# Kernel tuning notes

Hardware: AMD Instinct MI355X
Metric: run time of the kernel (lower is better)

Reference implementation:

```python
import jax, jax.numpy as jnp
import numpy as np

N_NODES = 50000
N_EDGES = 1_600_000
IN_C = 512
OUT_C = 10


def setup_inputs() -> dict:
    key = jax.random.key(0)
    ks = jax.random.split(key, 12)

    def glorot(k, fan_in, fan_out):
        lim = float(np.sqrt(6.0 / (fan_in + fan_out)))
        return jax.random.uniform(k, (fan_in, fan_out), jnp.float32, -lim, lim)

    x = jax.random.normal(ks[0], (N_NODES, IN_C), jnp.float32)
    edge_index = jax.random.randint(ks[1], (2, N_EDGES), 0, N_NODES, dtype=jnp.int64)
    return {
        "x": x,
        "edge_index": edge_index,
        "W1": glorot(ks[2], IN_C, 1024), "b1": jnp.zeros((1024,), jnp.float32),
        "W2": glorot(ks[3], 1024, 512), "b2": jnp.zeros((512,), jnp.float32),
        "W3": glorot(ks[4], 512, 128), "b3": jnp.zeros((128,), jnp.float32),
        "Wfc": glorot(ks[5], 128, OUT_C), "bfc": jnp.zeros((OUT_C,), jnp.float32),
    }


def gcn_conv(x, W, b, src, dst, norm, num_nodes):
    # GCNConv: out = D^{-1/2} (A + I) D^{-1/2} X W + b
    xw = x @ W  # [N, out_c]
    msg = xw[src] * norm[:, None]  # gather + scale per edge (incl. self-loops)
    out = jax.ops.segment_sum(msg, dst, num_segments=num_nodes)
    return out + b


def _build_sym_norm(edge_index, num_nodes):
    # add self-loops, compute symmetric normalization (PyG default gcn_norm)
    loop = jnp.arange(num_nodes, dtype=edge_index.dtype)
    src = jnp.concatenate([edge_index[0], loop])
    dst = jnp.concatenate([edge_index[1], loop])
    deg = jax.ops.segment_sum(jnp.ones_like(dst, dtype=jnp.float32), dst,
                              num_segments=num_nodes)
    dinv = jax.lax.rsqrt(jnp.maximum(deg, 1.0))  # deg >= 1 due to self-loops
    norm = dinv[src] * dinv[dst]
    return src, dst, norm


def reference(x, edge_index, W1, b1, W2, b2, W3, b3, Wfc, bfc):
    src, dst, norm = _build_sym_norm(edge_index, N_NODES)
    h = jax.nn.relu(gcn_conv(x, W1, b1, src, dst, norm, N_NODES))
    h = jax.nn.relu(gcn_conv(h, W2, b2, src, dst, norm, N_NODES))
    h = jax.nn.relu(gcn_conv(h, W3, b3, src, dst, norm, N_NODES))
    logits = h @ Wfc + bfc
    return jax.nn.log_softmax(logits, axis=1)
```

## Files before the change

### kernel.cpp

```cpp
#include <hip/hip_runtime.h>
#include <hip/hip_fp16.h>
#include <cstddef>

#define NN 50000
#define EE 1600000

typedef unsigned short ushortT;
typedef short bf16x8 __attribute__((ext_vector_type(8)));
typedef float f32x4 __attribute__((ext_vector_type(4)));
typedef unsigned short us8 __attribute__((ext_vector_type(8)));

struct h2x2 { __half2 a, b; };

__device__ __forceinline__ ushortT f2bf(float x) {
    unsigned u = __float_as_uint(x);
    u += 0x7fffu + ((u >> 16) & 1u);
    return (ushortT)(u >> 16);
}
__device__ __forceinline__ float bf2f(ushortT h) { return __uint_as_float(((unsigned)h) << 16); }

__global__ void detect_i64_kernel(const int* __restrict__ ei, int* __restrict__ flag) {
    __shared__ int any;
    if (threadIdx.x == 0) any = 0;
    __syncthreads();
    for (int i = threadIdx.x; i < 8192; i += 256)
        if (ei[2 * i + 1] != 0) any = 1;
    __syncthreads();
    if (threadIdx.x == 0) *flag = (any ? 0 : 1);
}

__global__ void canon_count_kernel(const int* __restrict__ ei, const int* __restrict__ flag,
                                   int* __restrict__ src32, int* __restrict__ dst32,
                                   unsigned* __restrict__ counts) {
    int e = blockIdx.x * blockDim.x + threadIdx.x;
    if (e >= EE) return;
    int s, d;
    if (*flag) {
        s = ei[2 * e];
        d = ei[2 * (EE + e)];
    } else {
        s = ei[e];
        d = ei[EE + e];
    }
    src32[e] = s;
    dst32[e] = d;
    atomicAdd(&counts[d], 1u);
}

__global__ void scan_part_kernel(const unsigned* __restrict__ counts, unsigned* __restrict__ part, int n) {
    __shared__ unsigned s[256];
    int i = blockIdx.x * 256 + threadIdx.x;
    s[threadIdx.x] = (i < n) ? counts[i] : 0u;
    __syncthreads();
    for (int off = 128; off > 0; off >>= 1) {
        if (threadIdx.x < (unsigned)off) s[threadIdx.x] += s[threadIdx.x + off];
        __syncthreads();
    }
    if (threadIdx.x == 0) part[blockIdx.x] = s[0];
}

__global__ void scan_base_kernel(unsigned* __restrict__ part, int nb) {
    __shared__ unsigned s[256];
    int t = threadIdx.x;
    unsigned v = (t < nb) ? part[t] : 0u;
    s[t] = v;
    __syncthreads();
    for (int off = 1; off < 256; off <<= 1) {
        unsigned a = (t >= off) ? s[t - off] : 0u;
        __syncthreads();
        s[t] += a;
        __syncthreads();
    }
    if (t < nb) part[t] = s[t] - v;
}

__global__ void scan_final_kernel(const unsigned* __restrict__ counts, const unsigned* __restrict__ part,
                                  unsigned* __restrict__ row_ptr, unsigned* __restrict__ cursor,
                                  float* __restrict__ dinv, int n) {
    __shared__ unsigned s[256];
    int b = blockIdx.x, t = threadIdx.x;
    int i = b * 256 + t;
    unsigned v = (i < n) ? counts[i] : 0u;
    s[t] = v;
    __syncthreads();
    for (int off = 1; off < 256; off <<= 1) {
        unsigned a = (t >= off) ? s[t - off] : 0u;
        __syncthreads();
        s[t] += a;
        __syncthreads();
    }
    if (i < n) {
        unsigned incl = s[t] + part[b];
        row_ptr[i + 1] = incl;
        cursor[i] = incl - v;
        dinv[i] = rsqrtf((float)v + 1.0f);
    }
    if (i == 0) row_ptr[0] = 0;
}

__global__ void scatter_kernel(const int* __restrict__ src, const int* __restrict__ dst,
                               const float* __restrict__ dinv, unsigned* __restrict__ cursor,
                               uint2* __restrict__ ed) {
    int e = blockIdx.x * blockDim.x + threadIdx.x;
    if (e >= EE) return;
    int d = dst[e], s = src[e];
    unsigned p = atomicAdd(&cursor[d], 1u);
    uint2 r;
    r.x = (unsigned)s;
    r.y = __float_as_uint(dinv[s] * dinv[d]);
    ed[p] = r;
}

__global__ void f32_to_f16_kernel(const float* __restrict__ in, __half* __restrict__ out, int n4) {
    int i = blockIdx.x * 256 + threadIdx.x;
    if (i >= n4) return;
    float4 v = ((const float4*)in)[i];
    h2x2 o;
    o.a = __floats2half2_rn(v.x, v.y);
    o.b = __floats2half2_rn(v.z, v.w);
    ((h2x2*)out)[i] = o;
}

__global__ void wconv_kernel(const float* __restrict__ W, ushortT* __restrict__ WTh,
                             ushortT* __restrict__ WTl, int K, int N) {
    int idx = blockIdx.x * 256 + threadIdx.x;
    if (idx >= K * N) return;
    int k = idx / N, n = idx - k * N;
    float w = W[idx];
    ushortT h = f2bf(w);
    ushortT l = f2bf(w - bf2f(h));
    WTh[(size_t)n * K + k] = h;
    WTl[(size_t)n * K + k] = l;
}

template <int RELU, int BIAS>
__global__ void aggregate512_kernel(const __half* __restrict__ F,
                                    ushortT* __restrict__ Oh, ushortT* __restrict__ Ol,
                                    const unsigned* __restrict__ row_ptr, const uint2* __restrict__ ed,
                                    const float* __restrict__ dinv, const float* __restrict__ bias) {
    int node = blockIdx.x;
    int t = threadIdx.x;
    float di = dinv[node];
    float dsl = di * di;
    h2x2 sv = ((const h2x2*)(F + (size_t)node * 512))[t];
    float2 s0 = __half22float2(sv.a), s1 = __half22float2(sv.b);
    float4 acc;
    acc.x = dsl * s0.x; acc.y = dsl * s0.y; acc.z = dsl * s1.x; acc.w = dsl * s1.y;
    unsigned k = row_ptr[node], end = row_ptr[node + 1];
    for (; k + 8 <= end; k += 8) {
        uint2 e[8];
#pragma unroll
        for (int j = 0; j < 8; j++) e[j] = ed[k + j];
        h2x2 f[8];
#pragma unroll
        for (int j = 0; j < 8; j++) f[j] = ((const h2x2*)(F + (size_t)e[j].x * 512))[t];
#pragma unroll
        for (int j = 0; j < 8; j++) {
            float w = __uint_as_float(e[j].y);
            float2 f0 = __half22float2(f[j].a), f1 = __half22float2(f[j].b);
            acc.x += w * f0.x;
            acc.y += w * f0.y;
            acc.z += w * f1.x;
            acc.w += w * f1.y;
        }
    }
    for (; k < end; k++) {
        uint2 e = ed[k];
        float w = __uint_as_float(e.y);
        h2x2 fv = ((const h2x2*)(F + (size_t)e.x * 512))[t];
        float2 f0 = __half22float2(fv.a), f1 = __half22float2(fv.b);
        acc.x += w * f0.x; acc.y += w * f0.y; acc.z += w * f1.x; acc.w += w * f1.y;
    }
    if (BIAS) {
        float4 bv = ((const float4*)bias)[t];
        acc.x += bv.x; acc.y += bv.y; acc.z += bv.z; acc.w += bv.w;
    }
    if (RELU) {
        acc.x = fmaxf(acc.x, 0.f); acc.y = fmaxf(acc.y, 0.f);
        acc.z = fmaxf(acc.z, 0.f); acc.w = fmaxf(acc.w, 0.f);
    }
    ushort4 h, l;
    h.x = f2bf(acc.x); l.x = f2bf(acc.x - bf2f(h.x));
    h.y = f2bf(acc.y); l.y = f2bf(acc.y - bf2f(h.y));
    h.z = f2bf(acc.z); l.z = f2bf(acc.z - bf2f(h.z));
    h.w = f2bf(acc.w); l.w = f2bf(acc.w - bf2f(h.w));
    ((ushort4*)(Oh + (size_t)node * 512))[t] = h;
    ((ushort4*)(Ol + (size_t)node * 512))[t] = l;
}

template <int RELU, int BIAS>
__global__ void aggregate128_kernel(const __half* __restrict__ F, float* __restrict__ O,
                                    const unsigned* __restrict__ row_ptr, const uint2* __restrict__ ed,
                                    const float* __restrict__ dinv, const float* __restrict__ bias) {
    int wid = threadIdx.x >> 6;
    int lane = threadIdx.x & 63;
    int node = blockIdx.x * 4 + wid;
    if (node >= NN) return;
    float di = dinv[node];
    float dsl = di * di;
    __half2 sv = ((const __half2*)(F + (size_t)node * 128))[lane];
    float2 sf = __half22float2(sv);
    float2 acc;
    acc.x = dsl * sf.x; acc.y = dsl * sf.y;
    unsigned k = row_ptr[node], end = row_ptr[node + 1];
    for (; k + 8 <= end; k += 8) {
        uint2 e[8];
#pragma unroll
        for (int j = 0; j < 8; j++) e[j] = ed[k + j];
        __half2 f[8];
#pragma unroll
        for (int j = 0; j < 8; j++) f[j] = ((const __half2*)(F + (size_t)e[j].x * 128))[lane];
#pragma unroll
        for (int j = 0; j < 8; j++) {
            float w = __uint_as_float(e[j].y);
            float2 ff = __half22float2(f[j]);
            acc.x += w * ff.x;
            acc.y += w * ff.y;
        }
    }
    for (; k < end; k++) {
        uint2 e = ed[k];
        float w = __uint_as_float(e.y);
        float2 ff = __half22float2(((const __half2*)(F + (size_t)e.x * 128))[lane]);
        acc.x += w * ff.x; acc.y += w * ff.y;
    }
    if (BIAS) {
        float2 bv = ((const float2*)bias)[lane];
        acc.x += bv.x; acc.y += bv.y;
    }
    if (RELU) { acc.x = fmaxf(acc.x, 0.f); acc.y = fmaxf(acc.y, 0.f); }
    ((float2*)(O + (size_t)node * 128))[lane] = acc;
}

template <int OUTMODE, int RELU, int BIAS>
__global__ __launch_bounds__(256) void gemm_mfma_kernel(
    const ushortT* __restrict__ Ah, const ushortT* __restrict__ Al,
    const ushortT* __restrict__ Bh, const ushortT* __restrict__ Bl,
    const float* __restrict__ bias,
    float* __restrict__ Cf, ushortT* __restrict__ Ch, ushortT* __restrict__ Cl,
    __half* __restrict__ Cg,
    int M, int N, int K) {
    __shared__ ushortT As[2][128][40];
    __shared__ ushortT Bs[2][128][40];
    int tid = threadIdx.x;
    int lane = tid & 63, wave = tid >> 6;
    int wr = wave >> 1, wc = wave & 1;

    int nx = gridDim.x;
    int nwg = nx * gridDim.y;
    int flat = blockIdx.x + nx * blockIdx.y;
    int q = nwg >> 3, r = nwg & 7;
    int xcd = flat & 7, pos = flat >> 3;
    int start = (xcd < r) ? xcd * (q + 1) : r * (q + 1) + (xcd - r) * q;
    int g = start + pos;
    int bm = (g / nx) * 128, bn = (g % nx) * 128;

    int srow = tid >> 1;
    int shalf = (tid & 1) * 16;
    int kg = lane >> 4, lr = lane & 15;

    f32x4 zero4 = {0.f, 0.f, 0.f, 0.f};
    f32x4 acc[4][4];
#pragma unroll
    for (int i = 0; i < 4; i++)
#pragma unroll
        for (int j = 0; j < 4; j++) acc[i][j] = zero4;

    int gm_st = bm + srow;
    const ushortT* pAh = Ah + (size_t)gm_st * K + shalf;
    const ushortT* pAl = Al + (size_t)gm_st * K + shalf;
    const ushortT* pBh = Bh + (size_t)(bn + srow) * K + shalf;
    const ushortT* pBl = Bl + (size_t)(bn + srow) * K + shalf;

    us8 z8 = {0,0,0,0,0,0,0,0};
    us8 ah0 = z8, ah1 = z8, al0 = z8, al1 = z8;
    us8 bh0, bh1, bl0, bl1;
    if (gm_st < M) {
        ah0 = *(const us8*)(pAh);
        ah1 = *(const us8*)(pAh + 8);
        al0 = *(const us8*)(pAl);
        al1 = *(const us8*)(pAl + 8);
    }
    bh0 = *(const us8*)(pBh);
    bh1 = *(const us8*)(pBh + 8);
    bl0 = *(const us8*)(pBl);
    bl1 = *(const us8*)(pBl + 8);

    for (int k0 = 0; k0 < K; k0 += 32) {
        __syncthreads();
        *(us8*)&As[0][srow][shalf] = ah0;
        *(us8*)&As[0][srow][shalf + 8] = ah1;
        *(us8*)&As[1][srow][shalf] = al0;
        *(us8*)&As[1][srow][shalf + 8] = al1;
        *(us8*)&Bs[0][srow][shalf] = bh0;
        *(us8*)&Bs[0][srow][shalf + 8] = bh1;
        *(us8*)&Bs[1][srow][shalf] = bl0;
        *(us8*)&Bs[1][srow][shalf + 8] = bl1;
        __syncthreads();

        int kn = k0 + 32;
        if (kn < K) {
            ah0 = ah1 = al0 = al1 = z8;
            if (gm_st < M) {
                ah0 = *(const us8*)(pAh + kn);
                ah1 = *(const us8*)(pAh + kn + 8);
                al0 = *(const us8*)(pAl + kn);
                al1 = *(const us8*)(pAl + kn + 8);
            }
            bh0 = *(const us8*)(pBh + kn);
            bh1 = *(const us8*)(pBh + kn + 8);
            bl0 = *(const us8*)(pBl + kn);
            bl1 = *(const us8*)(pBl + kn + 8);
        }

        bf16x8 afh[4], afl[4], bfh[4], bfl[4];
#pragma unroll
        for (int i = 0; i < 4; i++) {
            int rr = wr * 64 + i * 16 + lr;
            afh[i] = *(const bf16x8*)&As[0][rr][kg * 8];
            afl[i] = *(const bf16x8*)&As[1][rr][kg * 8];
        }
#pragma unroll
        for (int j = 0; j < 4; j++) {
            int c = wc * 64 + j * 16 + lr;
            bfh[j] = *(const bf16x8*)&Bs[0][c][kg * 8];
            bfl[j] = *(const bf16x8*)&Bs[1][c][kg * 8];
        }
#pragma unroll
        for (int i = 0; i < 4; i++)
#pragma unroll
            for (int j = 0; j < 4; j++) {
                acc[i][j] = __builtin_amdgcn_mfma_f32_16x16x32_bf16(afh[i], bfh[j], acc[i][j], 0, 0, 0);
                acc[i][j] = __builtin_amdgcn_mfma_f32_16x16x32_bf16(afh[i], bfl[j], acc[i][j], 0, 0, 0);
                acc[i][j] = __builtin_amdgcn_mfma_f32_16x16x32_bf16(afl[i], bfh[j], acc[i][j], 0, 0, 0);
            }
    }

#pragma unroll
    for (int i = 0; i < 4; i++)
#pragma unroll
        for (int j = 0; j < 4; j++) {
            int gn = bn + wc * 64 + j * 16 + lr;
            float bv = BIAS ? bias[gn] : 0.f;
#pragma unroll
            for (int reg = 0; reg < 4; reg++) {
                int gm = bm + wr * 64 + i * 16 + kg * 4 + reg;
                if (gm < M) {
                    float v = acc[i][j][reg] + bv;
                    if (RELU) v = fmaxf(v, 0.f);
                    if (OUTMODE == 0) {
                        Cf[(size_t)gm * N + gn] = v;
                    } else if (OUTMODE == 1) {
                        ushortT h = f2bf(v);
                        Ch[(size_t)gm * N + gn] = h;
                        Cl[(size_t)gm * N + gn] = f2bf(v - bf2f(h));
                    } else {
                        Cg[(size_t)gm * N + gn] = __float2half_rn(v);
                    }
                }
            }
        }
}

__global__ void fc_logsoftmax_kernel(const float* __restrict__ H, const float* __restrict__ Wfc,
                                     const float* __restrict__ bfc, float* __restrict__ out, int M) {
    int wid = threadIdx.x >> 6;
    int lane = threadIdx.x & 63;
    int node = blockIdx.x * 4 + wid;
    if (node >= M) return;
    const float* h = H + (size_t)node * 128;
    float d0 = h[lane], d1 = h[lane + 64];
    float lg[10];
#pragma unroll
    for (int c = 0; c < 10; c++) {
        float s = d0 * Wfc[lane * 10 + c] + d1 * Wfc[(lane + 64) * 10 + c];
#pragma unroll
        for (int o = 1; o < 64; o <<= 1) s += __shfl_xor(s, o, 64);
        lg[c] = s + bfc[c];
    }
    float mx = lg[0];
#pragma unroll
    for (int c = 1; c < 10; c++) mx = fmaxf(mx, lg[c]);
    float se = 0.f;
#pragma unroll
    for (int c = 0; c < 10; c++) se += expf(lg[c] - mx);
    float lse = logf(se) + mx;
    if (lane < 10) {
        float v = 0.f;
#pragma unroll
        for (int c = 0; c < 10; c++)
            if (lane == c) v = lg[c];
        out[(size_t)node * 10 + lane] = v - lse;
    }
}

extern "C" void kernel_launch(void* const* d_in, const int* in_sizes, int n_in,
                              void* d_out, int out_size, void* d_ws, size_t ws_size,
                              hipStream_t stream) {
    const float* x   = (const float*)d_in[0];
    const int*   ei  = (const int*)d_in[1];
    const float* W1  = (const float*)d_in[2];
    const float* b1  = (const float*)d_in[3];
    const float* W2  = (const float*)d_in[4];
    const float* b2  = (const float*)d_in[5];
    const float* W3  = (const float*)d_in[6];
    const float* b3  = (const float*)d_in[7];
    const float* Wfc = (const float*)d_in[8];
    const float* bfc = (const float*)d_in[9];
    float* out = (float*)d_out;

    char* ws = (char*)d_ws;
    size_t off = 0;
    auto alloc = [&](size_t bytes) -> void* {
        void* p = ws + off;
        off = (off + bytes + 255) & ~(size_t)255;
        return p;
    };
    int*      flag    = (int*)alloc(4);
    unsigned* counts  = (unsigned*)alloc((size_t)NN * 4);
    unsigned* row_ptr = (unsigned*)alloc((size_t)(NN + 1) * 4);
    unsigned* cursor  = (unsigned*)alloc((size_t)NN * 4);
    unsigned* part    = (unsigned*)alloc((size_t)256 * 4);
    float*    dinv    = (float*)alloc((size_t)NN * 4);
    int*      src32   = (int*)alloc((size_t)EE * 4);
    int*      dst32   = (int*)alloc((size_t)EE * 4);
    uint2*    ed      = (uint2*)alloc((size_t)EE * 8);
    ushortT*  W1Th    = (ushortT*)alloc((size_t)1024 * 512 * 2);
    ushortT*  W1Tl    = (ushortT*)alloc((size_t)1024 * 512 * 2);
    ushortT*  W2Th    = (ushortT*)alloc((size_t)512 * 1024 * 2);
    ushortT*  W2Tl    = (ushortT*)alloc((size_t)512 * 1024 * 2);
    ushortT*  W3Th    = (ushortT*)alloc((size_t)128 * 512 * 2);
    ushortT*  W3Tl    = (ushortT*)alloc((size_t)128 * 512 * 2);
    char*     bufA    = (char*)alloc((size_t)NN * 1024 * 2 * 2);
    char*     bufB    = (char*)alloc((size_t)NN * 512 * 4);

    __half*  xh  = (__half*)(bufA + (size_t)NN * 1024 * 2);
    ushortT* P1h = (ushortT*)bufB;
    ushortT* P1l = P1h + (size_t)NN * 512;
    ushortT* Q1h = (ushortT*)bufA;
    ushortT* Q1l = Q1h + (size_t)NN * 1024;
    __half*  G2h16 = (__half*)bufB;
    ushortT* P2h = (ushortT*)bufA;
    ushortT* P2l = P2h + (size_t)NN * 512;
    __half*  G3h16 = (__half*)bufB;
    float*   D2  = (float*)bufA;

    wconv_kernel<<<(512 * 1024 + 255) / 256, 256, 0, stream>>>(W1, W1Th, W1Tl, 512, 1024);
    wconv_kernel<<<(1024 * 512 + 255) / 256, 256, 0, stream>>>(W2, W2Th, W2Tl, 1024, 512);
    wconv_kernel<<<(512 * 128 + 255) / 256, 256, 0, stream>>>(W3, W3Th, W3Tl, 512, 128);

    hipMemsetAsync(counts, 0, (size_t)NN * 4, stream);
    detect_i64_kernel<<<1, 256, 0, stream>>>(ei, flag);
    canon_count_kernel<<<(EE + 255) / 256, 256, 0, stream>>>(ei, flag, src32, dst32, counts);
    const int NB = (NN + 255) / 256;
    scan_part_kernel<<<NB, 256, 0, stream>>>(counts, part, NN);
    scan_base_kernel<<<1, 256, 0, stream>>>(part, NB);
    scan_final_kernel<<<NB, 256, 0, stream>>>(counts, part, row_ptr, cursor, dinv, NN);
    scatter_kernel<<<(EE + 255) / 256, 256, 0, stream>>>(src32, dst32, dinv, cursor, ed);

    const int GY = (NN + 127) / 128;

    f32_to_f16_kernel<<<(NN * 512 / 4 + 255) / 256, 256, 0, stream>>>(x, xh, NN * 512 / 4);
    aggregate512_kernel<0, 0><<<NN, 128, 0, stream>>>(xh, P1h, P1l, row_ptr, ed, dinv, nullptr);
    gemm_mfma_kernel<1, 1, 1><<<dim3(1024 / 128, GY), 256, 0, stream>>>(
        P1h, P1l, W1Th, W1Tl, b1, nullptr, Q1h, Q1l, nullptr, NN, 1024, 512);

    gemm_mfma_kernel<2, 0, 0><<<dim3(512 / 128, GY), 256, 0, stream>>>(
        Q1h, Q1l, W2Th, W2Tl, nullptr, nullptr, nullptr, nullptr, G2h16, NN, 512, 1024);
    aggregate512_kernel<1, 1><<<NN, 128, 0, stream>>>(G2h16, P2h, P2l, row_ptr, ed, dinv, b2);

    gemm_mfma_kernel<2, 0, 0><<<dim3(128 / 128, GY), 256, 0, stream>>>(
        P2h, P2l, W3Th, W3Tl, nullptr, nullptr, nullptr, nullptr, G3h16, NN, 128, 512);
    aggregate128_kernel<1, 1><<<(NN + 3) / 4, 256, 0, stream>>>(G3h16, D2, row_ptr, ed, dinv, b3);

    fc_logsoftmax_kernel<<<(NN + 3) / 4, 256, 0, stream>>>(D2, Wfc, bfc, out, NN);
}
```

Before: 1.356 ms.

## Fuse final aggregation with FC+log-softmax and XOR-swizzle GEMM shared memory

Merges the 128-wide aggregation kernel with the final linear layer and log-softmax, so the intermediate fp32 activations are never written to and re-read from global memory and one launch is dropped. Separately, the GEMM shared-memory tiles lose their 40-element padding and use an XOR swizzle of 16-byte chunks instead, aiming to avoid LDS bank conflicts while using less shared memory. The fused kernel drops the node bounds check, which relies on NN being divisible by 4, and reads Wfc with a different lane-to-channel mapping.

```diff
diff --git a/kernel.cpp b/kernel.cpp
--- a/kernel.cpp
+++ b/kernel.cpp
@@ -188,14 +188,14 @@
     ((ushort4*)(Ol + (size_t)node * 512))[t] = l;
 }
 
-template <int RELU, int BIAS>
-__global__ void aggregate128_kernel(const __half* __restrict__ F, float* __restrict__ O,
+__global__ void agg128_fc_ls_kernel(const __half* __restrict__ F,
                                     const unsigned* __restrict__ row_ptr, const uint2* __restrict__ ed,
-                                    const float* __restrict__ dinv, const float* __restrict__ bias) {
+                                    const float* __restrict__ dinv, const float* __restrict__ bias,
+                                    const float* __restrict__ Wfc, const float* __restrict__ bfc,
+                                    float* __restrict__ out) {
     int wid = threadIdx.x >> 6;
     int lane = threadIdx.x & 63;
     int node = blockIdx.x * 4 + wid;
-    if (node >= NN) return;
     float di = dinv[node];
     float dsl = di * di;
     __half2 sv = ((const __half2*)(F + (size_t)node * 128))[lane];
@@ -224,12 +224,31 @@
         float2 ff = __half22float2(((const __half2*)(F + (size_t)e.x * 128))[lane]);
         acc.x += w * ff.x; acc.y += w * ff.y;
     }
-    if (BIAS) {
-        float2 bv = ((const float2*)bias)[lane];
-        acc.x += bv.x; acc.y += bv.y;
-    }
-    if (RELU) { acc.x = fmaxf(acc.x, 0.f); acc.y = fmaxf(acc.y, 0.f); }
-    ((float2*)(O + (size_t)node * 128))[lane] = acc;
+    float2 bv = ((const float2*)bias)[lane];
+    acc.x = fmaxf(acc.x + bv.x, 0.f);
+    acc.y = fmaxf(acc.y + bv.y, 0.f);
+    float lg[10];
+#pragma unroll
+    for (int c = 0; c < 10; c++) {
+        float s = acc.x * Wfc[(2 * lane) * 10 + c] + acc.y * Wfc[(2 * lane + 1) * 10 + c];
+#pragma unroll
+        for (int o = 1; o < 64; o <<= 1) s += __shfl_xor(s, o, 64);
+        lg[c] = s + bfc[c];
+    }
+    float mx = lg[0];
+#pragma unroll
+    for (int c = 1; c < 10; c++) mx = fmaxf(mx, lg[c]);
+    float se = 0.f;
+#pragma unroll
+    for (int c = 0; c < 10; c++) se += expf(lg[c] - mx);
+    float lse = logf(se) + mx;
+    if (lane < 10) {
+        float v = 0.f;
+#pragma unroll
+        for (int c = 0; c < 10; c++)
+            if (lane == c) v = lg[c];
+        out[(size_t)node * 10 + lane] = v - lse;
+    }
 }
 
 template <int OUTMODE, int RELU, int BIAS>
@@ -240,8 +259,8 @@
     float* __restrict__ Cf, ushortT* __restrict__ Ch, ushortT* __restrict__ Cl,
     __half* __restrict__ Cg,
     int M, int N, int K) {
-    __shared__ ushortT As[2][128][40];
-    __shared__ ushortT Bs[2][128][40];
+    __shared__ ushortT As[2][128][32];
+    __shared__ ushortT Bs[2][128][32];
     int tid = threadIdx.x;
     int lane = tid & 63, wave = tid >> 6;
     int wr = wave >> 1, wc = wave & 1;
@@ -256,8 +275,12 @@
     int bm = (g / nx) * 128, bn = (g % nx) * 128;
 
     int srow = tid >> 1;
-    int shalf = (tid & 1) * 16;
+    int sh = tid & 1;
     int kg = lane >> 4, lr = lane & 15;
+
+    int wsz = ((srow >> 3) & 1) << 1;
+    int wc0 = (2 * sh + 0) ^ wsz;
+    int wc1 = (2 * sh + 1) ^ wsz;
 
     f32x4 zero4 = {0.f, 0.f, 0.f, 0.f};
     f32x4 acc[4][4];
@@ -267,6 +290,7 @@
         for (int j = 0; j < 4; j++) acc[i][j] = zero4;
 
     int gm_st = bm + srow;
+    int shalf = sh * 16;
     const ushortT* pAh = Ah + (size_t)gm_st * K + shalf;
     const ushortT* pAl = Al + (size_t)gm_st * K + shalf;
     const ushortT* pBh = Bh + (size_t)(bn + srow) * K + shalf;
@@ -288,14 +312,14 @@
 
     for (int k0 = 0; k0 < K; k0 += 32) {
         __syncthreads();
-        *(us8*)&As[0][srow][shalf] = ah0;
-        *(us8*)&As[0][srow][shalf + 8] = ah1;
-        *(us8*)&As[1][srow][shalf] = al0;
-        *(us8*)&As[1][srow][shalf + 8] = al1;
-        *(us8*)&Bs[0][srow][shalf] = bh0;
-        *(us8*)&Bs[0][srow][shalf + 8] = bh1;
-        *(us8*)&Bs[1][srow][shalf] = bl0;
-        *(us8*)&Bs[1][srow][shalf + 8] = bl1;
+        *(us8*)&As[0][srow][wc0 * 8] = ah0;
+        *(us8*)&As[0][srow][wc1 * 8] = ah1;
+        *(us8*)&As[1][srow][wc0 * 8] = al0;
+        *(us8*)&As[1][srow][wc1 * 8] = al1;
+        *(us8*)&Bs[0][srow][wc0 * 8] = bh0;
+        *(us8*)&Bs[0][srow][wc1 * 8] = bh1;
+        *(us8*)&Bs[1][srow][wc0 * 8] = bl0;
+        *(us8*)&Bs[1][srow][wc1 * 8] = bl1;
         __syncthreads();
 
         int kn = k0 + 32;
@@ -317,14 +341,16 @@
 #pragma unroll
         for (int i = 0; i < 4; i++) {
             int rr = wr * 64 + i * 16 + lr;
-            afh[i] = *(const bf16x8*)&As[0][rr][kg * 8];
-            afl[i] = *(const bf16x8*)&As[1][rr][kg * 8];
+            int ck = (kg ^ (((rr >> 3) & 1) << 1)) * 8;
+            afh[i] = *(const bf16x8*)&As[0][rr][ck];
+            afl[i] = *(const bf16x8*)&As[1][rr][ck];
         }
 #pragma unroll
         for (int j = 0; j < 4; j++) {
-            int c = wc * 64 + j * 16 + lr;
-            bfh[j] = *(const bf16x8*)&Bs[0][c][kg * 8];
-            bfl[j] = *(const bf16x8*)&Bs[1][c][kg * 8];
+            int cc = wc * 64 + j * 16 + lr;
+            int ck = (kg ^ (((cc >> 3) & 1) << 1)) * 8;
+            bfh[j] = *(const bf16x8*)&Bs[0][cc][ck];
+            bfl[j] = *(const bf16x8*)&Bs[1][cc][ck];
         }
 #pragma unroll
         for (int i = 0; i < 4; i++)
@@ -360,38 +386,6 @@
                 }
             }
         }
-}
-
-__global__ void fc_logsoftmax_kernel(const float* __restrict__ H, const float* __restrict__ Wfc,
-                                     const float* __restrict__ bfc, float* __restrict__ out, int M) {
-    int wid = threadIdx.x >> 6;
-    int lane = threadIdx.x & 63;
-    int node = blockIdx.x * 4 + wid;
-    if (node >= M) return;
-    const float* h = H + (size_t)node * 128;
-    float d0 = h[lane], d1 = h[lane + 64];
-    float lg[10];
-#pragma unroll
-    for (int c = 0; c < 10; c++) {
-        float s = d0 * Wfc[lane * 10 + c] + d1 * Wfc[(lane + 64) * 10 + c];
-#pragma unroll
-        for (int o = 1; o < 64; o <<= 1) s += __shfl_xor(s, o, 64);
-        lg[c] = s + bfc[c];
-    }
-    float mx = lg[0];
-#pragma unroll
-    for (int c = 1; c < 10; c++) mx = fmaxf(mx, lg[c]);
-    float se = 0.f;
-#pragma unroll
-    for (int c = 0; c < 10; c++) se += expf(lg[c] - mx);
-    float lse = logf(se) + mx;
-    if (lane < 10) {
-        float v = 0.f;
-#pragma unroll
-        for (int c = 0; c < 10; c++)
-            if (lane == c) v = lg[c];
-        out[(size_t)node * 10 + lane] = v - lse;
-    }
 }
 
 extern "C" void kernel_launch(void* const* d_in, const int* in_sizes, int n_in,
@@ -443,7 +437,6 @@
     ushortT* P2h = (ushortT*)bufA;
     ushortT* P2l = P2h + (size_t)NN * 512;
     __half*  G3h16 = (__half*)bufB;
-    float*   D2  = (float*)bufA;
 
     wconv_kernel<<<(512 * 1024 + 255) / 256, 256, 0, stream>>>(W1, W1Th, W1Tl, 512, 1024);
     wconv_kernel<<<(1024 * 512 + 255) / 256, 256, 0, stream>>>(W2, W2Th, W2Tl, 1024, 512);
@@ -471,7 +464,5 @@
 
     gemm_mfma_kernel<2, 0, 0><<<dim3(128 / 128, GY), 256, 0, stream>>>(
         P2h, P2l, W3Th, W3Tl, nullptr, nullptr, nullptr, nullptr, G3h16, NN, 128, 512);
-    aggregate128_kernel<1, 1><<<(NN + 3) / 4, 256, 0, stream>>>(G3h16, D2, row_ptr, ed, dinv, b3);
-
-    fc_logsoftmax_kernel<<<(NN + 3) / 4, 256, 0, stream>>>(D2, Wfc, bfc, out, NN);
-}
+    agg128_fc_ls_kernel<<<NN / 4, 256, 0, stream>>>(G3h16, row_ptr, ed, dinv, b3, Wfc, bfc, out);
+}
```

New measurement: 1.311 ms. 1.03x faster.
